# Optimization experiments

Hardware: AMD Instinct MI355X
Metric: run time of the kernel (lower is better)

Reference implementation:

```python
import jax, jax.numpy as jnp
import numpy as np

S = 2048      # sequence length (prefill, start_idx=0)
D = 4096      # model dim
H = 32        # query heads
KVH = 8       # kv heads (GQA)
HD = D // H   # head dim = 128
ROPE_BASE = 500000.0  # llama3 rope theta
NEG = -1e9    # additive causal mask value (finite stand-in for -inf)


def setup_inputs() -> dict:
    key = jax.random.key(0)
    ks = jax.random.split(key, 5)
    scale = 1.0 / np.sqrt(D)
    x = jax.random.normal(ks[0], (S, D), jnp.float32)
    wq = jax.random.normal(ks[1], (D, D), jnp.float32) * scale
    wk = jax.random.normal(ks[2], (KVH * HD, D), jnp.float32) * scale
    wv = jax.random.normal(ks[3], (KVH * HD, D), jnp.float32) * scale
    wo = jax.random.normal(ks[4], (D, D), jnp.float32) * scale
    # RoPE tables, [S, HD//2]
    pos = jnp.arange(S, dtype=jnp.float32)
    inv_freq = 1.0 / (ROPE_BASE ** (jnp.arange(0, HD, 2, dtype=jnp.float32) / HD))
    ang = pos[:, None] * inv_freq[None, :]
    freqs_cos = jnp.cos(ang)
    freqs_sin = jnp.sin(ang)
    # additive causal mask [S, S]
    mask = jnp.where(jnp.tril(jnp.ones((S, S), bool)), 0.0, NEG).astype(jnp.float32)
    return dict(x=x, wq=wq, wk=wk, wv=wv, wo=wo, mask=mask,
                freqs_cos=freqs_cos, freqs_sin=freqs_sin)


def _rope(t, cos, sin):
    # t: [S, nh, hd]; cos/sin: [S, hd//2] -> interleaved even/odd rotation
    even = t[:, :, 0::2]
    odd = t[:, :, 1::2]
    c = cos[:, None, :]
    s = sin[:, None, :]
    re = even * c - odd * s
    im = even * s + odd * c
    return jnp.stack([re, im], axis=-1).reshape(t.shape)


def reference(x, wq, wk, wv, wo, mask, freqs_cos, freqs_sin):
    s, d = x.shape
    q = (x @ wq.T).reshape(s, H, HD)
    k = (x @ wk.T).reshape(s, KVH, HD)
    v = (x @ wv.T).reshape(s, KVH, HD)
    q = _rope(q, freqs_cos, freqs_sin)
    k = _rope(k, freqs_cos, freqs_sin)
    # KV-cache append at start_idx=0 then read back == identity (prefill)
    # GQA: repeat_interleave kv heads to match query heads
    k = jnp.repeat(k, H // KVH, axis=1)  # [s, H, HD]
    v = jnp.repeat(v, H // KVH, axis=1)
    logits = jnp.einsum('qhd,khd->hqk', q, k) * (1.0 / np.sqrt(HD)) + mask[None]
    p = jax.nn.softmax(logits, axis=-1)
    o = jnp.einsum('hqk,khd->qhd', p, v).reshape(s, d)
    return o @ wo.T
```

## Files before the change

### kernel.cpp

```cpp
#include <hip/hip_runtime.h>
#include <hip/hip_bf16.h>
#include <stdint.h>

#define S2   2048
#define DD   4096
#define NH   32
#define NKVH 8
#define HD2  128
#define QKVW 6144

typedef __bf16 bf16x8 __attribute__((ext_vector_type(8)));
typedef float  f32x4  __attribute__((ext_vector_type(4)));
typedef unsigned short u16x8 __attribute__((ext_vector_type(8)));
typedef unsigned short u16x4 __attribute__((ext_vector_type(4)));

__device__ __forceinline__ unsigned short f2b(float f) {
    unsigned int u = __builtin_bit_cast(unsigned int, f);
    unsigned int r = (u + 0x7FFFu + ((u >> 16) & 1u)) >> 16;
    return (unsigned short)r;
}
__device__ __forceinline__ float b2f(unsigned short h) {
    unsigned int u = ((unsigned int)h) << 16;
    return __builtin_bit_cast(float, u);
}
__device__ __forceinline__ unsigned cvt_pk_bf16(float a, float b) {
    unsigned r;
    asm("v_cvt_pk_bf16_f32 %0, %1, %2" : "=v"(r) : "v"(a), "v"(b));
    return r;
}

__device__ __forceinline__ void gload_lds16(const void* g, void* lds) {
    __builtin_amdgcn_global_load_lds(
        (const __attribute__((address_space(1))) void*)(uintptr_t)g,
        (__attribute__((address_space(3))) void*)(uint32_t)(uintptr_t)lds,
        16, 0, 0);
}

#define BAR() do { asm volatile("" ::: "memory"); \
                   __builtin_amdgcn_s_barrier();  \
                   asm volatile("" ::: "memory"); } while (0)
#define WAITV(n) asm volatile("s_waitcnt vmcnt(" #n ")" ::: "memory")

template<int N> __device__ __forceinline__ void waitv() {
    if      constexpr (N == 0)  WAITV(0);
    else if constexpr (N == 1)  WAITV(1);
    else if constexpr (N == 2)  WAITV(2);
    else if constexpr (N == 3)  WAITV(3);
    else if constexpr (N == 4)  WAITV(4);
    else if constexpr (N == 5)  WAITV(5);
    else if constexpr (N == 6)  WAITV(6);
    else if constexpr (N == 8)  WAITV(8);
}

__global__ void cvt_all(const float* __restrict__ x,  const float* __restrict__ wq,
                        const float* __restrict__ wk, const float* __restrict__ wv,
                        unsigned short* __restrict__ dst) {
    const long long NG = 8LL * 1024 * 1024;
    const long long stride = (long long)gridDim.x * blockDim.x;
    for (long long g = (long long)blockIdx.x * blockDim.x + threadIdx.x; g < NG; g += stride) {
        const float* src; long long off;
        if      (g < 2LL*1024*1024) { src = x;  off = g; }
        else if (g < 6LL*1024*1024) { src = wq; off = g - 2LL*1024*1024; }
        else if (g < 7LL*1024*1024) { src = wk; off = g - 6LL*1024*1024; }
        else                        { src = wv; off = g - 7LL*1024*1024; }
        f32x4 v = *reinterpret_cast<const f32x4*>(src + off * 4);
        u16x4 o;
        o[0] = f2b(v[0]); o[1] = f2b(v[1]); o[2] = f2b(v[2]); o[3] = f2b(v[3]);
        *reinterpret_cast<u16x4*>(dst + g * 4) = o;
    }
}

__global__ __launch_bounds__(512) void gemm_qkv(
    const unsigned short* __restrict__ A,
    const unsigned short* __restrict__ B0,
    const unsigned short* __restrict__ B1,
    const unsigned short* __restrict__ B2,
    unsigned short* __restrict__ C)
{
    constexpr int K = 4096, BK = 64, NT = K / BK;
    __shared__ unsigned short As[2][256 * 64];
    __shared__ unsigned short Bs[2][192 * 64];

    const int bm = blockIdx.y, bn = blockIdx.x;
    const int tid = threadIdx.x;
    const int w = tid >> 6, lane = tid & 63;
    const int wr = w >> 1, wc = w & 1;
    const int r16 = lane & 15, g4 = lane >> 4;

    const int bn0 = bn * 192;
    const unsigned short* Ap = A + (size_t)bm * 256 * K;

    const int lrow = lane >> 3;
    const int lchk = lane & 7;

    f32x4 acc[4][6] = {};
    bf16x8 af[2][2], b0[3][2], b1[3][2];

    auto browbase = [&](int rowg) -> const unsigned short* {
        if (rowg < 4096) return B0 + (size_t)rowg * K;
        if (rowg < 5120) return B1 + (size_t)(rowg - 4096) * K;
        return B2 + (size_t)(rowg - 5120) * K;
    };

    auto stageA = [&](int buf, int tt, int half) {
        #pragma unroll
        for (int i = 0; i < 2; ++i) {
            const int j = i * 8 + w;
            const int row0 = (j >> 2) * 64 + half * 32 + (j & 3) * 8;
            const int row = row0 + lrow;
            gload_lds16(Ap + (size_t)row * K + tt * BK + ((lchk ^ (row & 7)) * 8),
                        &As[buf][row0 * 64]);
        }
    };
    auto stageB = [&](int buf, int tt, int half) {
        #pragma unroll
        for (int i = 0; i < 2; ++i) {
            const int j = (i == 0) ? w : (8 + (w & 3));
            const int row0 = (j < 6) ? (half * 48 + j * 8)
                                     : (96 + half * 48 + (j - 6) * 8);
            const int row = row0 + lrow;
            const unsigned short* src = browbase(bn0 + row0) + (size_t)lrow * K;
            gload_lds16(src + tt * BK + ((lchk ^ (row & 7)) * 8),
                        &Bs[buf][row0 * 64]);
        }
    };
    auto readA = [&](int buf, int mh) {
        #pragma unroll
        for (int m = 0; m < 2; ++m)
            #pragma unroll
            for (int kk = 0; kk < 2; ++kk) {
                const int row = wr * 64 + mh * 32 + m * 16 + r16;
                af[m][kk] = *reinterpret_cast<const bf16x8*>(
                    &As[buf][row * 64 + (((kk * 4 + g4) ^ (row & 7)) * 8)]);
            }
    };
    auto readB = [&](int buf, int nh, bf16x8 (&br)[3][2]) {
        #pragma unroll
        for (int n = 0; n < 3; ++n)
            #pragma unroll
            for (int kk = 0; kk < 2; ++kk) {
                const int row = wc * 96 + nh * 48 + n * 16 + r16;
                br[n][kk] = *reinterpret_cast<const bf16x8*>(
                    &Bs[buf][row * 64 + (((kk * 4 + g4) ^ (row & 7)) * 8)]);
            }
    };
    auto mma = [&](bf16x8 (&br)[3][2], int mh, int nh) {
        __builtin_amdgcn_s_setprio(1);
        #pragma unroll
        for (int m = 0; m < 2; ++m)
            #pragma unroll
            for (int n = 0; n < 3; ++n)
                #pragma unroll
                for (int kk = 0; kk < 2; ++kk)
                    acc[mh * 2 + m][nh * 3 + n] = __builtin_amdgcn_mfma_f32_16x16x32_bf16(
                        af[m][kk], br[n][kk], acc[mh * 2 + m][nh * 3 + n], 0, 0, 0);
        __builtin_amdgcn_s_setprio(0);
    };

    stageA(0, 0, 0); stageB(0, 0, 0); stageB(0, 0, 1); stageA(0, 0, 1);
    waitv<4>();
    BAR();

    for (int t = 0; t < NT - 1; ++t) {
        const int buf = t & 1;
        readA(buf, 0); readB(buf, 0, b0);
        stageA(buf ^ 1, t + 1, 0); stageB(buf ^ 1, t + 1, 0);
        BAR();
        mma(b0, 0, 0);
        waitv<6>();
        BAR();
        readB(buf, 1, b1);
        stageB(buf ^ 1, t + 1, 1);
        BAR();
        mma(b1, 0, 1);
        waitv<6>();
        BAR();
        readA(buf, 1);
        stageA(buf ^ 1, t + 1, 1);
        BAR();
        mma(b1, 1, 1);
        BAR();
        mma(b0, 1, 0);
        waitv<4>();
        BAR();
    }
    {
        const int buf = (NT - 1) & 1;
        readA(buf, 0); readB(buf, 0, b0);
        BAR();
        mma(b0, 0, 0);
        waitv<2>();
        BAR();
        readB(buf, 1, b1);
        mma(b1, 0, 1);
        waitv<0>();
        readA(buf, 1);
        mma(b1, 1, 1);
        mma(b0, 1, 0);
    }

    const size_t crow0 = (size_t)bm * 256 + wr * 64;
    const size_t ccol0 = (size_t)bn0 + wc * 96;
    #pragma unroll
    for (int m = 0; m < 4; ++m)
        #pragma unroll
        for (int n = 0; n < 6; ++n)
            #pragma unroll
            for (int r = 0; r < 4; ++r)
                C[(crow0 + m * 16 + g4 * 4 + r) * QKVW + ccol0 + n * 16 + r16] =
                    f2b(acc[m][n][r]);
}

__global__ __launch_bounds__(512) void gemm_out(
    const unsigned short* __restrict__ A,
    const unsigned short* __restrict__ B,
    float* __restrict__ C)
{
    constexpr int K = 4096, BK = 64, NT = K / BK;
    __shared__ unsigned short As[2][128 * 64];
    __shared__ unsigned short Bs[2][256 * 64];

    const int bm = blockIdx.y, bn = blockIdx.x;
    const int tid = threadIdx.x;
    const int w = tid >> 6, lane = tid & 63;
    const int wr = w >> 2, wc = w & 3;
    const int r16 = lane & 15, g4 = lane >> 4;

    const unsigned short* Ap = A + (size_t)bm * 128 * K;
    const unsigned short* Bp = B + (size_t)bn * 256 * K;

    const int lrow = lane >> 3;
    const int lchk = lane & 7;

    f32x4 acc[4][4] = {};
    bf16x8 af[2][2], b0[2][2], b1[2][2];

    auto stageA = [&](int buf, int tt, int half) {
        const int j = w;
        const int row0 = (j >> 2) * 64 + half * 32 + (j & 3) * 8;
        const int row = row0 + lrow;
        gload_lds16(Ap + (size_t)row * K + tt * BK + ((lchk ^ (row & 7)) * 8),
                    &As[buf][row0 * 64]);
    };
    auto stageB = [&](int buf, int tt, int half) {
        #pragma unroll
        for (int i = 0; i < 2; ++i) {
            const int j = i * 8 + w;
            const int row0 = (j >> 2) * 64 + half * 32 + (j & 3) * 8;
            const int row = row0 + lrow;
            gload_lds16(Bp + (size_t)row * K + tt * BK + ((lchk ^ (row & 7)) * 8),
                        &Bs[buf][row0 * 64]);
        }
    };
    auto readA = [&](int buf, int mh) {
        #pragma unroll
        for (int m = 0; m < 2; ++m)
            #pragma unroll
            for (int kk = 0; kk < 2; ++kk) {
                const int row = wr * 64 + mh * 32 + m * 16 + r16;
                af[m][kk] = *reinterpret_cast<const bf16x8*>(
                    &As[buf][row * 64 + (((kk * 4 + g4) ^ (row & 7)) * 8)]);
            }
    };
    auto readB = [&](int buf, int nh, bf16x8 (&br)[2][2]) {
        #pragma unroll
        for (int n = 0; n < 2; ++n)
            #pragma unroll
            for (int kk = 0; kk < 2; ++kk) {
                const int row = wc * 64 + nh * 32 + n * 16 + r16;
                br[n][kk] = *reinterpret_cast<const bf16x8*>(
                    &Bs[buf][row * 64 + (((kk * 4 + g4) ^ (row & 7)) * 8)]);
            }
    };
    auto mma = [&](bf16x8 (&br)[2][2], int mh, int nh) {
        __builtin_amdgcn_s_setprio(1);
        #pragma unroll
        for (int m = 0; m < 2; ++m)
            #pragma unroll
            for (int n = 0; n < 2; ++n)
                #pragma unroll
                for (int kk = 0; kk < 2; ++kk)
                    acc[mh * 2 + m][nh * 2 + n] = __builtin_amdgcn_mfma_f32_16x16x32_bf16(
                        af[m][kk], br[n][kk], acc[mh * 2 + m][nh * 2 + n], 0, 0, 0);
        __builtin_amdgcn_s_setprio(0);
    };

    stageA(0, 0, 0); stageB(0, 0, 0); stageB(0, 0, 1); stageA(0, 0, 1);
    waitv<3>();
    BAR();

    for (int t = 0; t < NT - 1; ++t) {
        const int buf = t & 1;
        readA(buf, 0); readB(buf, 0, b0);
        stageA(buf ^ 1, t + 1, 0); stageB(buf ^ 1, t + 1, 0);
        BAR();
        mma(b0, 0, 0);
        waitv<4>();
        BAR();
        readB(buf, 1, b1);
        stageB(buf ^ 1, t + 1, 1);
        BAR();
        mma(b1, 0, 1);
        waitv<5>();
        BAR();
        readA(buf, 1);
        stageA(buf ^ 1, t + 1, 1);
        BAR();
        mma(b1, 1, 1);
        BAR();
        mma(b0, 1, 0);
        waitv<3>();
        BAR();
    }
    {
        const int buf = (NT - 1) & 1;
        readA(buf, 0); readB(buf, 0, b0);
        BAR();
        mma(b0, 0, 0);
        waitv<1>();
        BAR();
        readB(buf, 1, b1);
        mma(b1, 0, 1);
        waitv<0>();
        readA(buf, 1);
        mma(b1, 1, 1);
        mma(b0, 1, 0);
    }

    const size_t crow0 = (size_t)bm * 128 + wr * 64;
    const size_t ccol0 = (size_t)bn * 256 + wc * 64;
    #pragma unroll
    for (int m = 0; m < 4; ++m)
        #pragma unroll
        for (int n = 0; n < 4; ++n)
            #pragma unroll
            for (int r = 0; r < 4; ++r)
                C[(crow0 + m * 16 + g4 * 4 + r) * DD + ccol0 + n * 16 + r16] = acc[m][n][r];
}

__global__ __launch_bounds__(256) void rope_tv(unsigned short* __restrict__ qkv,
                                               const float* __restrict__ fc,
                                               const float* __restrict__ fs,
                                               unsigned short* __restrict__ Vt) {
    __shared__ unsigned short tile[64][72];
    const int bid = blockIdx.x;
    if (bid < 6144) {
        constexpr float QSCALE = 0.08838834764831845f * 1.4426950408889634f;
        const int g = (bid % 3) * 256 + threadIdx.x;
        if (g >= 640) return;
        const int s = bid / 3;
        const int col = g * 8;
        unsigned short* p = qkv + (size_t)s * QKVW + col;
        u16x8 v = *reinterpret_cast<const u16x8*>(p);
        const int i0 = (col & 127) >> 1;
        f32x4 c  = *reinterpret_cast<const f32x4*>(fc + s * 64 + i0);
        f32x4 sn = *reinterpret_cast<const f32x4*>(fs + s * 64 + i0);
        const float post = (col < DD) ? QSCALE : 1.0f;
        u16x8 o;
        #pragma unroll
        for (int j = 0; j < 4; ++j) {
            float e  = b2f(v[2*j]);
            float od = b2f(v[2*j+1]);
            o[2*j]   = f2b((e * c[j] - od * sn[j]) * post);
            o[2*j+1] = f2b((e * sn[j] + od * c[j]) * post);
        }
        *reinterpret_cast<u16x8*>(p) = o;
    } else {
        const int t = bid - 6144;
        const int d0g = (t & 15) * 64;
        const int s0  = (t >> 4) * 64;
        const int kvh = d0g >> 7, dl0 = d0g & 127;
        const int tid = threadIdx.x;
        #pragma unroll
        for (int p = 0; p < 2; ++p) {
            const int sgi = p * 256 + tid;
            const int srow = sgi >> 3, dseg = sgi & 7;
            u16x8 v = *reinterpret_cast<const u16x8*>(
                qkv + (size_t)(s0 + srow) * QKVW + 5120 + d0g + dseg * 8);
            #pragma unroll
            for (int j = 0; j < 8; ++j) tile[srow][dseg * 8 + j] = v[j];
        }
        __syncthreads();
        #pragma unroll
        for (int p = 0; p < 2; ++p) {
            const int sgi = p * 256 + tid;
            const int drow = sgi >> 3, sseg = sgi & 7;
            u16x8 v;
            #pragma unroll
            for (int j = 0; j < 8; ++j) v[j] = tile[sseg * 8 + j][drow];
            *reinterpret_cast<u16x8*>(
                Vt + (size_t)kvh * HD2 * S2 + (size_t)(dl0 + drow) * S2 + s0 + sseg * 8) = v;
        }
    }
}

__global__ __launch_bounds__(512) void attn_kernel(const unsigned short* __restrict__ Qkv,
                                                   const unsigned short* __restrict__ Vt,
                                                   unsigned short* __restrict__ O,
                                                   const float* __restrict__ wo_src,
                                                   unsigned short* __restrict__ wo_dst) {
    __shared__ unsigned short Klds[2][64 * 128];
    __shared__ unsigned short Vlds[2][128 * 64];
    __shared__ unsigned short Plds[8][2048];

    const int kvh = blockIdx.x;
    const int h   = kvh * 4 + (blockIdx.y & 3);
    const int p   = blockIdx.y >> 2;
    const int cB  = 8 + p, cS = 7 - p;
    const int w = threadIdx.x >> 6, lane = threadIdx.x & 63;
    const int tid = threadIdx.x;
    const int r16 = lane & 15, g4 = lane >> 4;

    const int myc = (w < 4) ? cB : cS;
    const int qw  = myc * 128 + (w & 3) * 32;
    const int ntB = 2 * cB + 2;

    const unsigned short* Kbase = Qkv + DD + kvh * HD2;
    const unsigned short* Vtb   = Vt + (size_t)kvh * HD2 * S2;
    char* pw = (char*)(&Plds[w][0]);

    const int blk = blockIdx.y * 8 + blockIdx.x;
    const f32x4* wo4 = (const f32x4*)wo_src;
    const int cb4 = blk * 16384 + tid;
    f32x4 cbuf[2];
    auto cvt_issue = [&](int k) {
        #pragma unroll
        for (int i = 0; i < 2; ++i)
            cbuf[i] = wo4[cb4 + k * 1024 + i * 512];
    };
    auto cvt_flush = [&](int k) {
        #pragma unroll
        for (int i = 0; i < 2; ++i) {
            u16x4 ov;
            ov[0] = f2b(cbuf[i][0]); ov[1] = f2b(cbuf[i][1]);
            ov[2] = f2b(cbuf[i][2]); ov[3] = f2b(cbuf[i][3]);
            *reinterpret_cast<u16x4*>(wo_dst + ((size_t)(cb4 + k * 1024 + i * 512)) * 4) = ov;
        }
    };

    const int krow_l = lane >> 4;
    const int kchunk = lane & 15;
    const int vd_l   = lane >> 3;
    const int vchunk = lane & 7;

    bf16x8 qf[2][4];
    #pragma unroll
    for (int m = 0; m < 2; ++m)
        #pragma unroll
        for (int f = 0; f < 4; ++f)
            qf[m][f] = *reinterpret_cast<const bf16x8*>(
                Qkv + (size_t)(qw + m * 16 + r16) * QKVW + h * HD2 + f * 32 + g4 * 8);

    f32x4 o[2][8] = {};
    float mr[2] = {-3e38f, -3e38f};
    float lr[2] = {0.f, 0.f};

    auto stage = [&](int buf, int kv0) {
        #pragma unroll
        for (int i = 0; i < 2; ++i) {
            const int seg = i * 8 + w;
            const int row = seg * 4 + krow_l;
            gload_lds16(Kbase + (size_t)(kv0 + row) * QKVW + ((kchunk ^ (row & 7)) * 8),
                        &Klds[buf][seg * 512]);
        }
        #pragma unroll
        for (int i = 0; i < 2; ++i) {
            const int seg = i * 8 + w;
            const int d = seg * 8 + vd_l;
            gload_lds16(Vtb + (size_t)d * S2 + kv0 + ((vchunk ^ (d & 7)) * 8),
                        &Vlds[buf][seg * 512]);
        }
    };

    stage(0, 0);
    WAITV(0);
    __syncthreads();
    cvt_issue(0);

    for (int t = 0; t < ntB; ++t) {
        if (t >= 1 && t <= 16) {
            cvt_flush(t - 1);
            if (t < 16) cvt_issue(t);
        }
        const int buf = t & 1;
        const int kv0 = t * 64;
        if (t + 1 < ntB) stage(buf ^ 1, (t + 1) * 64);

        if (kv0 <= qw + 31) {
            f32x4 sa[2][4] = {};
            #pragma unroll
            for (int kb = 0; kb < 4; ++kb) {
                bf16x8 kf[4];
                #pragma unroll
                for (int f = 0; f < 4; ++f)
                    kf[f] = *reinterpret_cast<const bf16x8*>(
                        &Klds[buf][(kb * 16 + r16) * 128 + (((f * 4 + g4) ^ (r16 & 7)) * 8)]);
                __builtin_amdgcn_s_setprio(1);
                #pragma unroll
                for (int m = 0; m < 2; ++m)
                    #pragma unroll
                    for (int f = 0; f < 4; ++f)
                        sa[m][kb] = __builtin_amdgcn_mfma_f32_16x16x32_bf16(
                            kf[f], qf[m][f], sa[m][kb], 0, 0, 0);
                __builtin_amdgcn_s_setprio(0);
            }
            const bool needmask = (kv0 + 63 > qw);
            float sv[2][4][4];
            #pragma unroll
            for (int m = 0; m < 2; ++m)
                #pragma unroll
                for (int kb = 0; kb < 4; ++kb)
                    #pragma unroll
                    for (int r = 0; r < 4; ++r) {
                        float xx = sa[m][kb][r];
                        if (needmask) {
                            const int kvg = kv0 + kb * 16 + g4 * 4 + r;
                            const int qg  = qw + m * 16 + r16;
                            xx = (kvg > qg) ? -3e38f : xx;
                        }
                        sv[m][kb][r] = xx;
                    }
            float rowm[2];
            #pragma unroll
            for (int m = 0; m < 2; ++m) {
                float a0 = fmaxf(fmaxf(sv[m][0][0], sv[m][0][1]), fmaxf(sv[m][0][2], sv[m][0][3]));
                float a1 = fmaxf(fmaxf(sv[m][1][0], sv[m][1][1]), fmaxf(sv[m][1][2], sv[m][1][3]));
                float a2 = fmaxf(fmaxf(sv[m][2][0], sv[m][2][1]), fmaxf(sv[m][2][2], sv[m][2][3]));
                float a3 = fmaxf(fmaxf(sv[m][3][0], sv[m][3][1]), fmaxf(sv[m][3][2], sv[m][3][3]));
                rowm[m] = fmaxf(fmaxf(a0, a1), fmaxf(a2, a3));
            }
            #pragma unroll
            for (int m = 0; m < 2; ++m) {
                rowm[m] = fmaxf(rowm[m], __shfl_xor(rowm[m], 16));
                rowm[m] = fmaxf(rowm[m], __shfl_xor(rowm[m], 32));
            }
            const float gmax = fmaxf(rowm[0] - mr[0], rowm[1] - mr[1]);
            if (!__all(gmax <= 11.5f)) {
                float corr[2];
                #pragma unroll
                for (int m = 0; m < 2; ++m) {
                    const float mn = fmaxf(mr[m], rowm[m]);
                    corr[m] = exp2f(mr[m] - mn);
                    mr[m] = mn;
                    lr[m] *= corr[m];
                }
                #pragma unroll
                for (int m = 0; m < 2; ++m)
                    #pragma unroll
                    for (int r = 0; r < 4; ++r) {
                        const float co = __shfl(corr[m], (lane & 48) | (g4 * 4 + r));
                        #pragma unroll
                        for (int n = 0; n < 8; ++n) o[m][n][r] *= co;
                    }
            }
            float rs[2] = {0.f, 0.f};
            #pragma unroll
            for (int m = 0; m < 2; ++m)
                #pragma unroll
                for (int kb = 0; kb < 4; ++kb)
                    #pragma unroll
                    for (int r = 0; r < 4; ++r) {
                        const float pp = exp2f(sv[m][kb][r] - mr[m]);
                        sv[m][kb][r] = pp;
                        rs[m] += pp;
                    }
            #pragma unroll
            for (int m = 0; m < 2; ++m) {
                rs[m] += __shfl_xor(rs[m], 16);
                rs[m] += __shfl_xor(rs[m], 32);
                lr[m] += rs[m];
            }
            #pragma unroll
            for (int m = 0; m < 2; ++m)
                #pragma unroll
                for (int kb = 0; kb < 4; ++kb) {
                    const unsigned w0 = cvt_pk_bf16(sv[m][kb][0], sv[m][kb][1]);
                    const unsigned w1 = cvt_pk_bf16(sv[m][kb][2], sv[m][kb][3]);
                    int wa = m * 2048 + ((kb * 2) + (g4 >> 1)) * 256 + r16 * 16 + (g4 & 1) * 8;
                    wa ^= (r16 >> 3) << 4;
                    *reinterpret_cast<unsigned long long*>(pw + wa) =
                        (unsigned long long)w0 | ((unsigned long long)w1 << 32);
                }
            asm volatile("s_waitcnt lgkmcnt(0)" ::: "memory");
            bf16x8 pa[2][2];
            #pragma unroll
            for (int m = 0; m < 2; ++m)
                #pragma unroll
                for (int kvs = 0; kvs < 2; ++kvs) {
                    int ra = m * 2048 + kvs * 1024 + lane * 16;
                    ra ^= (r16 >> 3) << 4;
                    pa[m][kvs] = *reinterpret_cast<const bf16x8*>(pw + ra);
                }
            #pragma unroll
            for (int kvs = 0; kvs < 2; ++kvs)
                #pragma unroll
                for (int n = 0; n < 8; ++n) {
                    const bf16x8 vb = *reinterpret_cast<const bf16x8*>(
                        &Vlds[buf][(n * 16 + r16) * 64 + (((kvs * 4 + g4) ^ (r16 & 7)) * 8)]);
                    __builtin_amdgcn_s_setprio(1);
                    #pragma unroll
                    for (int m = 0; m < 2; ++m)
                        o[m][n] = __builtin_amdgcn_mfma_f32_16x16x32_bf16(
                            pa[m][kvs], vb, o[m][n], 0, 0, 0);
                    __builtin_amdgcn_s_setprio(0);
                }
        }

        WAITV(0);
        __syncthreads();
    }

    float inv[2];
    #pragma unroll
    for (int m = 0; m < 2; ++m) inv[m] = 1.0f / lr[m];
    #pragma unroll
    for (int m = 0; m < 2; ++m)
        #pragma unroll
        for (int r = 0; r < 4; ++r) {
            const float iv = __shfl(inv[m], (lane & 48) | (g4 * 4 + r));
            #pragma unroll
            for (int n = 0; n < 8; ++n)
                O[(size_t)(qw + m * 16 + g4 * 4 + r) * DD + h * HD2 + n * 16 + r16] =
                    f2b(o[m][n][r] * iv);
        }
}

extern "C" void kernel_launch(void* const* d_in, const int* in_sizes, int n_in,
                              void* d_out, int out_size, void* d_ws, size_t ws_size,
                              hipStream_t stream) {
    (void)in_sizes; (void)n_in; (void)out_size; (void)ws_size;
    const float* x  = (const float*)d_in[0];
    const float* wq = (const float*)d_in[1];
    const float* wk = (const float*)d_in[2];
    const float* wv = (const float*)d_in[3];
    const float* wo = (const float*)d_in[4];
    const float* fc = (const float*)d_in[6];
    const float* fs = (const float*)d_in[7];
    float* out = (float*)d_out;

    unsigned short* ws = (unsigned short*)d_ws;
    const size_t M1 = 1024 * 1024;
    unsigned short* xb  = ws;
    unsigned short* wqb = ws + 8  * M1;
    unsigned short* wkb = ws + 24 * M1;
    unsigned short* wvb = ws + 28 * M1;
    unsigned short* wob = ws + 32 * M1;
    unsigned short* qkv = ws + 48 * M1;
    unsigned short* vt  = ws + 60 * M1;
    unsigned short* ob  = ws + 62 * M1;

    cvt_all<<<2048, 256, 0, stream>>>(x, wq, wk, wv, ws);
    gemm_qkv<<<dim3(32, 8), 512, 0, stream>>>(xb, wqb, wkb, wvb, qkv);
    rope_tv<<<6656, 256, 0, stream>>>(qkv, fc, fs, vt);
    attn_kernel<<<dim3(8, 32), 512, 0, stream>>>(qkv, vt, ob, wo, wob);
    gemm_out<<<dim3(16, 16), 512, 0, stream>>>(ob, wob, out);
}
```

Before: 288.7 us.

## Restructure GEMM main loops into two phases with fewer barriers

```diff
diff --git a/kernel.cpp b/kernel.cpp
--- a/kernel.cpp
+++ b/kernel.cpp
@@ -94,7 +94,7 @@
     const int lchk = lane & 7;
 
     f32x4 acc[4][6] = {};
-    bf16x8 af[2][2], b0[3][2], b1[3][2];
+    bf16x8 af[4][2], b0[3][2], b1[3][2];
 
     auto browbase = [&](int rowg) -> const unsigned short* {
         if (rowg < 4096) return B0 + (size_t)rowg * K;
@@ -130,7 +130,7 @@
             #pragma unroll
             for (int kk = 0; kk < 2; ++kk) {
                 const int row = wr * 64 + mh * 32 + m * 16 + r16;
-                af[m][kk] = *reinterpret_cast<const bf16x8*>(
+                af[mh * 2 + m][kk] = *reinterpret_cast<const bf16x8*>(
                     &As[buf][row * 64 + (((kk * 4 + g4) ^ (row & 7)) * 8)]);
             }
     };
@@ -144,59 +144,44 @@
                     &Bs[buf][row * 64 + (((kk * 4 + g4) ^ (row & 7)) * 8)]);
             }
     };
-    auto mma = [&](bf16x8 (&br)[3][2], int mh, int nh) {
+    auto mma = [&](bf16x8 (&br)[3][2], int nh) {
         __builtin_amdgcn_s_setprio(1);
         #pragma unroll
-        for (int m = 0; m < 2; ++m)
+        for (int m = 0; m < 4; ++m)
             #pragma unroll
             for (int n = 0; n < 3; ++n)
                 #pragma unroll
                 for (int kk = 0; kk < 2; ++kk)
-                    acc[mh * 2 + m][nh * 3 + n] = __builtin_amdgcn_mfma_f32_16x16x32_bf16(
-                        af[m][kk], br[n][kk], acc[mh * 2 + m][nh * 3 + n], 0, 0, 0);
+                    acc[m][nh * 3 + n] = __builtin_amdgcn_mfma_f32_16x16x32_bf16(
+                        af[m][kk], br[n][kk], acc[m][nh * 3 + n], 0, 0, 0);
         __builtin_amdgcn_s_setprio(0);
     };
 
-    stageA(0, 0, 0); stageB(0, 0, 0); stageB(0, 0, 1); stageA(0, 0, 1);
-    waitv<4>();
+    stageA(0, 0, 0); stageA(0, 0, 1); stageB(0, 0, 0); stageB(0, 0, 1);
+    waitv<0>();
     BAR();
 
     for (int t = 0; t < NT - 1; ++t) {
         const int buf = t & 1;
-        readA(buf, 0); readB(buf, 0, b0);
-        stageA(buf ^ 1, t + 1, 0); stageB(buf ^ 1, t + 1, 0);
-        BAR();
-        mma(b0, 0, 0);
+        readA(buf, 0); readA(buf, 1); readB(buf, 0, b0);
+        stageA(buf ^ 1, t + 1, 0); stageA(buf ^ 1, t + 1, 1); stageB(buf ^ 1, t + 1, 0);
+        mma(b0, 0);
         waitv<6>();
         BAR();
         readB(buf, 1, b1);
         stageB(buf ^ 1, t + 1, 1);
-        BAR();
-        mma(b1, 0, 1);
-        waitv<6>();
-        BAR();
-        readA(buf, 1);
-        stageA(buf ^ 1, t + 1, 1);
-        BAR();
-        mma(b1, 1, 1);
-        BAR();
-        mma(b0, 1, 0);
-        waitv<4>();
+        mma(b1, 1);
+        waitv<2>();
         BAR();
     }
     {
         const int buf = (NT - 1) & 1;
-        readA(buf, 0); readB(buf, 0, b0);
-        BAR();
-        mma(b0, 0, 0);
-        waitv<2>();
+        readA(buf, 0); readA(buf, 1); readB(buf, 0, b0);
+        mma(b0, 0);
+        waitv<0>();
         BAR();
         readB(buf, 1, b1);
-        mma(b1, 0, 1);
-        waitv<0>();
-        readA(buf, 1);
-        mma(b1, 1, 1);
-        mma(b0, 1, 0);
+        mma(b1, 1);
     }
 
     const size_t crow0 = (size_t)bm * 256 + wr * 64;
@@ -233,7 +218,7 @@
     const int lchk = lane & 7;
 
     f32x4 acc[4][4] = {};
-    bf16x8 af[2][2], b0[2][2], b1[2][2];
+    bf16x8 af[4][2], b0[2][2], b1[2][2];
 
     auto stageA = [&](int buf, int tt, int half) {
         const int j = w;
@@ -258,7 +243,7 @@
             #pragma unroll
             for (int kk = 0; kk < 2; ++kk) {
                 const int row = wr * 64 + mh * 32 + m * 16 + r16;
-                af[m][kk] = *reinterpret_cast<const bf16x8*>(
+                af[mh * 2 + m][kk] = *reinterpret_cast<const bf16x8*>(
                     &As[buf][row * 64 + (((kk * 4 + g4) ^ (row & 7)) * 8)]);
             }
     };
@@ -272,59 +257,44 @@
                     &Bs[buf][row * 64 + (((kk * 4 + g4) ^ (row & 7)) * 8)]);
             }
     };
-    auto mma = [&](bf16x8 (&br)[2][2], int mh, int nh) {
+    auto mma = [&](bf16x8 (&br)[2][2], int nh) {
         __builtin_amdgcn_s_setprio(1);
         #pragma unroll
-        for (int m = 0; m < 2; ++m)
+        for (int m = 0; m < 4; ++m)
             #pragma unroll
             for (int n = 0; n < 2; ++n)
                 #pragma unroll
                 for (int kk = 0; kk < 2; ++kk)
-                    acc[mh * 2 + m][nh * 2 + n] = __builtin_amdgcn_mfma_f32_16x16x32_bf16(
-                        af[m][kk], br[n][kk], acc[mh * 2 + m][nh * 2 + n], 0, 0, 0);
+                    acc[m][nh * 2 + n] = __builtin_amdgcn_mfma_f32_16x16x32_bf16(
+                        af[m][kk], br[n][kk], acc[m][nh * 2 + n], 0, 0, 0);
         __builtin_amdgcn_s_setprio(0);
     };
 
-    stageA(0, 0, 0); stageB(0, 0, 0); stageB(0, 0, 1); stageA(0, 0, 1);
-    waitv<3>();
+    stageA(0, 0, 0); stageA(0, 0, 1); stageB(0, 0, 0); stageB(0, 0, 1);
+    waitv<0>();
     BAR();
 
     for (int t = 0; t < NT - 1; ++t) {
         const int buf = t & 1;
-        readA(buf, 0); readB(buf, 0, b0);
-        stageA(buf ^ 1, t + 1, 0); stageB(buf ^ 1, t + 1, 0);
-        BAR();
-        mma(b0, 0, 0);
+        readA(buf, 0); readA(buf, 1); readB(buf, 0, b0);
+        stageA(buf ^ 1, t + 1, 0); stageA(buf ^ 1, t + 1, 1); stageB(buf ^ 1, t + 1, 0);
+        mma(b0, 0);
         waitv<4>();
         BAR();
         readB(buf, 1, b1);
         stageB(buf ^ 1, t + 1, 1);
-        BAR();
-        mma(b1, 0, 1);
-        waitv<5>();
-        BAR();
-        readA(buf, 1);
-        stageA(buf ^ 1, t + 1, 1);
-        BAR();
-        mma(b1, 1, 1);
-        BAR();
-        mma(b0, 1, 0);
-        waitv<3>();
+        mma(b1, 1);
+        waitv<2>();
         BAR();
     }
     {
         const int buf = (NT - 1) & 1;
-        readA(buf, 0); readB(buf, 0, b0);
-        BAR();
-        mma(b0, 0, 0);
-        waitv<1>();
+        readA(buf, 0); readA(buf, 1); readB(buf, 0, b0);
+        mma(b0, 0);
+        waitv<0>();
         BAR();
         readB(buf, 1, b1);
-        mma(b1, 0, 1);
-        waitv<0>();
-        readA(buf, 1);
-        mma(b1, 1, 1);
-        mma(b0, 1, 0);
+        mma(b1, 1);
     }
 
     const size_t crow0 = (size_t)bm * 128 + wr * 64;
```

Result: faster. 282.0 us (-2.3%).
